# Kernel tuning notes

Hardware: AMD Instinct MI355X
Metric: run time of the kernel (lower is better)

The kernel has to match this reference:

```python
import jax, jax.numpy as jnp
import numpy as np

N_HEADS = 12


def setup_inputs() -> dict:
    key = jax.random.key(0)
    ks = jax.random.split(key, 3)
    B, N, C = 32, 1024, 768
    x = jax.random.normal(ks[0], (B, N, C), dtype=jnp.float32)
    w_qkv = jax.random.normal(ks[1], (C, 3 * C), dtype=jnp.float32) * (1.0 / np.sqrt(C))
    b_qkv = jnp.zeros((3 * C,), dtype=jnp.float32)
    w_out = jax.random.normal(ks[2], (C, C), dtype=jnp.float32) * (1.0 / np.sqrt(C))
    b_out = jnp.zeros((C,), dtype=jnp.float32)
    return {"x": x, "w_qkv": w_qkv, "b_qkv": b_qkv, "w_out": w_out, "b_out": b_out}


def reference(x, w_qkv, b_qkv, w_out, b_out):
    B, N, C = x.shape
    H = N_HEADS
    D = C // H  # head_dim
    qkv = (x @ w_qkv + b_qkv).reshape(B, N, 3, H, D)
    qkv = jnp.transpose(qkv, (2, 0, 3, 1, 4))
    q, k, v = qkv[0], qkv[1], qkv[2]
    # channel attention: k^T @ v -> (B,H,D,D), scaled by sqrt(head_dim)
    attn = jnp.einsum("bhnd,bhne->bhde", k, v) / np.sqrt(D).astype(np.float32)
    attn = jax.nn.softmax(attn, axis=-1)
    # attn @ q^T -> (B,H,D,N); swapaxes -> (B,H,N,D)
    out = jnp.einsum("bhde,bhne->bhnd", attn, q)
    # ProjOut: merge heads (B,N,C) + Dense(C)
    out = jnp.transpose(out, (0, 2, 1, 3)).reshape(B, N, C)
    return out @ w_out + b_out
```

## Files before the change

### kernel.cpp

```cpp
#include <hip/hip_runtime.h>
#include <hip/hip_bf16.h>
#include <stdint.h>
#include <stddef.h>

#define B_ 32
#define N_ 1024
#define C_ 768
#define H_ 12
#define D_ 64
#define M_ (B_*N_)
#define TC_ (3*C_)

typedef __bf16 bf16_t;
typedef __attribute__((ext_vector_type(8))) __bf16 bf16x8;
typedef __attribute__((ext_vector_type(4))) __bf16 bf16x4;
typedef __attribute__((ext_vector_type(4))) float  f32x4;
typedef __attribute__((ext_vector_type(16))) float f32x16;

#define MFMA16(a,b,c) __builtin_amdgcn_mfma_f32_16x16x32_bf16(a,b,c,0,0,0)
#define MFMA32(a,b,c) __builtin_amdgcn_mfma_f32_32x32x16_bf16(a,b,c,0,0,0)

__device__ __forceinline__ void lds_load16(const void* g, void* l) {
  __builtin_amdgcn_global_load_lds(
      (const __attribute__((address_space(1))) void*)g,
      (__attribute__((address_space(3))) void*)l, 16, 0, 0);
}

__global__ void cvt_bf16(const float* __restrict__ in, bf16_t* __restrict__ out, int n) {
  int i = (blockIdx.x * 256 + threadIdx.x) * 8;
  if (i >= n) return;
  const float4 a = *(const float4*)(in + i);
  const float4 b = *(const float4*)(in + i + 4);
  bf16x8 r;
  r[0]=(bf16_t)a.x; r[1]=(bf16_t)a.y; r[2]=(bf16_t)a.z; r[3]=(bf16_t)a.w;
  r[4]=(bf16_t)b.x; r[5]=(bf16_t)b.y; r[6]=(bf16_t)b.z; r[7]=(bf16_t)b.w;
  *(bf16x8*)(out + i) = r;
}

__global__ void transpose_cvt(const float* __restrict__ in, bf16_t* __restrict__ out,
                              int R, int Cc) {
  __shared__ float t[32][33];
  const int c0 = blockIdx.x * 32, r0 = blockIdx.y * 32;
  const int tx = threadIdx.x & 31, ty = threadIdx.x >> 5;
  #pragma unroll
  for (int k = 0; k < 4; ++k)
    t[ty + k*8][tx] = in[(size_t)(r0 + ty + k*8)*Cc + c0 + tx];
  __syncthreads();
  #pragma unroll
  for (int k = 0; k < 4; ++k)
    out[(size_t)(c0 + ty + k*8)*R + r0 + tx] = (bf16_t)t[tx][ty + k*8];
}

template<int MODE>
__global__ __launch_bounds__(256, 2)
void gemm_bt(const bf16_t* __restrict__ A, const bf16_t* __restrict__ BT,
             const float* __restrict__ bias, float* __restrict__ Cout,
             bf16_t* __restrict__ qh,
             bf16_t* __restrict__ kthi, bf16_t* __restrict__ vthi,
             int K, int nbx, size_t bt_bstride)
{
  __shared__ __align__(16) char smem[34816];
  bf16_t* As   = (bf16_t*)smem;
  bf16_t* Bs   = (bf16_t*)(smem + 8192);
  bf16_t* tile = (bf16_t*)smem;

  const int nwg = gridDim.x;
  const int cpx = nwg >> 3;
  const int bid = blockIdx.x;
  const int swz = (bid & 7) * cpx + (bid >> 3);
  const int bx  = swz % nbx;
  const int by  = swz / nbx;

  const int tid  = threadIdx.x;
  const int wave = tid >> 6;
  const int lane = tid & 63;
  const int rowBase = by * 128;
  const int colBase = bx * 128;
  const int wr = (wave >> 1) * 64;
  const int wc = (wave &  1) * 64;
  const int l31 = lane & 31;
  const int lhi = lane >> 5;
  const int xr  = (lane >> 1) & 3;
  const int r0t = tid >> 2;
  const int c0s = (((tid & 3) ^ ((tid >> 3) & 3)) << 3);

  const bf16_t* Bp = BT + (MODE == 3 ? (size_t)(rowBase >> 10) * bt_bstride : 0)
                        + (size_t)(colBase + r0t) * K + c0s;
  const bf16_t* Ap;
  if (MODE == 3) {
    const int gr = rowBase + r0t;
    Ap = A + (size_t)(gr >> 10) * (H_ * N_ * D_) + (size_t)(gr & (N_ - 1)) * D_ + c0s;
  } else {
    Ap = A + (size_t)(rowBase + r0t) * K + c0s;
  }

  f32x16 acc[2][2];
  #pragma unroll
  for (int m = 0; m < 2; ++m)
    #pragma unroll
    for (int n = 0; n < 2; ++n)
      #pragma unroll
      for (int j = 0; j < 16; ++j) acc[m][n][j] = 0.f;

  for (int k0 = 0; k0 < K; k0 += 32) {
    const bf16_t* a0;
    size_t a_half;
    if (MODE == 3) { a0 = Ap + (size_t)(k0 >> 6) * (N_ * D_) + (k0 & 63); a_half = (size_t)64 * D_; }
    else           { a0 = Ap + k0;                                        a_half = (size_t)64 * K;  }
    lds_load16(a0,              &As[wave * 512]);
    lds_load16(a0 + a_half,     &As[2048 + wave * 512]);
    lds_load16(Bp + k0,                  &Bs[wave * 512]);
    lds_load16(Bp + (size_t)64 * K + k0, &Bs[2048 + wave * 512]);
    __syncthreads();
    bf16x8 af[2][2], bfv[2][2];
    #pragma unroll
    for (int m = 0; m < 2; ++m)
      #pragma unroll
      for (int kk = 0; kk < 2; ++kk)
        af[m][kk] = *(const bf16x8*)&As[(wr + m*32 + l31)*32 + (((2*kk + lhi) ^ xr) << 3)];
    #pragma unroll
    for (int n = 0; n < 2; ++n)
      #pragma unroll
      for (int kk = 0; kk < 2; ++kk)
        bfv[n][kk] = *(const bf16x8*)&Bs[(wc + n*32 + l31)*32 + (((2*kk + lhi) ^ xr) << 3)];
    #pragma unroll
    for (int m = 0; m < 2; ++m)
      #pragma unroll
      for (int n = 0; n < 2; ++n)
        #pragma unroll
        for (int kk = 0; kk < 2; ++kk)
          acc[m][n] = MFMA32(af[m][kk], bfv[n][kk], acc[m][n]);
    __syncthreads();
  }

  if (MODE == 3) {
    #pragma unroll
    for (int n = 0; n < 2; ++n) {
      const int gc = colBase + wc + n*32 + l31;
      const float bb = bias[gc];
      #pragma unroll
      for (int m = 0; m < 2; ++m)
        #pragma unroll
        for (int g = 0; g < 4; ++g) {
          const int gr = rowBase + wr + m*32 + g*8 + lhi*4;
          #pragma unroll
          for (int j = 0; j < 4; ++j)
            Cout[(size_t)(gr + j)*C_ + gc] = acc[m][n][4*g + j] + bb;
        }
    }
  } else {
    #pragma unroll
    for (int n = 0; n < 2; ++n) {
      const int c  = wc + n*32 + l31;
      const float bb = bias[colBase + c];
      #pragma unroll
      for (int m = 0; m < 2; ++m)
        #pragma unroll
        for (int g = 0; g < 4; ++g) {
          const int r0 = wr + m*32 + g*8 + lhi*4;
          bf16x4 hv;
          hv[0]=(bf16_t)(acc[m][n][4*g+0]+bb); hv[1]=(bf16_t)(acc[m][n][4*g+1]+bb);
          hv[2]=(bf16_t)(acc[m][n][4*g+2]+bb); hv[3]=(bf16_t)(acc[m][n][4*g+3]+bb);
          *(bf16x4*)&tile[c*136 + r0] = hv;
        }
    }
    __syncthreads();
    const int s   = colBase / C_;
    const int b   = rowBase >> 10;
    const int nn0 = rowBase & (N_ - 1);
    if (s == 0) {
      const int r  = tid >> 1, ch = tid & 1;
      const int h  = (colBase >> 6) + ch;
      bf16_t* dst = qh + (((size_t)b*H_ + h)*N_ + nn0 + r)*D_;
      #pragma unroll
      for (int i0 = 0; i0 < 64; i0 += 8) {
        bf16x8 vv;
        #pragma unroll
        for (int i = 0; i < 8; ++i) vv[i] = tile[(ch*64 + i0 + i)*136 + r];
        *(bf16x8*)&dst[i0] = vv;
      }
    } else {
      const int c  = tid >> 1, rh = tid & 1;
      const int rem = colBase + c - s*C_;
      const int h = rem >> 6, d = rem & 63;
      bf16_t* dst = (s == 1 ? kthi : vthi)
                    + (((size_t)b*H_ + h)*D_ + d)*N_ + nn0 + rh*64;
      #pragma unroll
      for (int i0 = 0; i0 < 64; i0 += 8)
        *(bf16x8*)&dst[i0] = *(const bf16x8*)&tile[c*136 + rh*64 + i0];
    }
  }
}

__global__ __launch_bounds__(256, 2)
void attn_softmax_k(const bf16_t* __restrict__ kthi, const bf16_t* __restrict__ vthi,
                    bf16_t* __restrict__ attnT)
{
  __shared__ float tile[64][65];
  __shared__ float invs[64];
  const int bh = blockIdx.x;
  const int tid = threadIdx.x, wave = tid >> 6, lane = tid & 63;
  const int fr = lane & 15, fo = (lane >> 4) * 8;
  const size_t base = (size_t)bh * D_ * N_;
  f32x4 acc[4][4] = {{0.f,0.f,0.f,0.f}};
  const int k0lo = wave * 256;
  #pragma unroll 1
  for (int k0 = k0lo; k0 < k0lo + 256; k0 += 32) {
    bf16x8 ah[4], bhv[4];
    #pragma unroll
    for (int m = 0; m < 4; ++m)
      ah[m] = *(const bf16x8*)&kthi[base + (size_t)(m*16 + fr)*N_ + k0 + fo];
    #pragma unroll
    for (int n = 0; n < 4; ++n)
      bhv[n] = *(const bf16x8*)&vthi[base + (size_t)(n*16 + fr)*N_ + k0 + fo];
    #pragma unroll
    for (int m = 0; m < 4; ++m)
      #pragma unroll
      for (int n = 0; n < 4; ++n)
        acc[m][n] = MFMA16(ah[m], bhv[n], acc[m][n]);
  }
  for (int w = 0; w < 4; ++w) {
    if (wave == w) {
      #pragma unroll
      for (int m = 0; m < 4; ++m)
        #pragma unroll
        for (int n = 0; n < 4; ++n) {
          const int row = m*16 + ((lane >> 4) << 2);
          const int col = n*16 + fr;
          #pragma unroll
          for (int j = 0; j < 4; ++j) {
            if (w == 0) tile[row+j][col]  = acc[m][n][j];
            else        tile[row+j][col] += acc[m][n][j];
          }
        }
    }
    __syncthreads();
  }
  if (tid < 64) {
    float mx = -3.0e38f;
    #pragma unroll
    for (int c = 0; c < 64; ++c) mx = fmaxf(mx, tile[tid][c]);
    mx *= 0.125f;
    float ssum = 0.f;
    #pragma unroll
    for (int c = 0; c < 64; ++c) {
      const float ev = __expf(tile[tid][c]*0.125f - mx);
      tile[tid][c] = ev;
      ssum += ev;
    }
    invs[tid] = 1.0f / ssum;
  }
  __syncthreads();
  if (tid < 64) {
    bf16_t* ao = attnT + (size_t)bh * D_ * D_ + tid * D_;
    #pragma unroll
    for (int d0 = 0; d0 < 64; d0 += 8) {
      bf16x8 vv;
      #pragma unroll
      for (int i = 0; i < 8; ++i) vv[i] = (bf16_t)(tile[d0+i][tid] * invs[d0+i]);
      *(bf16x8*)&ao[d0] = vv;
    }
  }
}

__global__ __launch_bounds__(256, 2)
void compose_w2(const bf16_t* __restrict__ woutT, const bf16_t* __restrict__ attnT,
                bf16_t* __restrict__ w2t)
{
  const int jb = blockIdx.x;
  const int bh = blockIdx.y;
  const int b = bh / H_, h = bh - b*H_;
  const int tid = threadIdx.x, wave = tid >> 6, lane = tid & 63;
  const int fr = lane & 15, fo = (lane >> 4) * 8;
  const bf16_t* at = attnT + (size_t)bh * D_ * D_;
  f32x4 acc[2][4] = {{0.f,0.f,0.f,0.f}};
  #pragma unroll
  for (int kk = 0; kk < 2; ++kk) {
    bf16x8 af[2], bfv[4];
    #pragma unroll
    for (int m = 0; m < 2; ++m)
      af[m] = *(const bf16x8*)&woutT[(size_t)(jb*128 + wave*32 + m*16 + fr)*C_ + h*64 + kk*32 + fo];
    #pragma unroll
    for (int n = 0; n < 4; ++n)
      bfv[n] = *(const bf16x8*)&at[(n*16 + fr)*64 + kk*32 + fo];
    #pragma unroll
    for (int m = 0; m < 2; ++m)
      #pragma unroll
      for (int n = 0; n < 4; ++n)
        acc[m][n] = MFMA16(af[m], bfv[n], acc[m][n]);
  }
  bf16_t* wb = w2t + (size_t)b * C_ * C_;
  #pragma unroll
  for (int m = 0; m < 2; ++m) {
    const int j = jb*128 + wave*32 + m*16 + ((lane >> 4) << 2);
    #pragma unroll
    for (int n = 0; n < 4; ++n) {
      const int e = n*16 + fr;
      #pragma unroll
      for (int jj = 0; jj < 4; ++jj)
        wb[(size_t)(j + jj)*C_ + h*64 + e] = (bf16_t)acc[m][n][jj];
    }
  }
}

extern "C" void kernel_launch(void* const* d_in, const int* in_sizes, int n_in,
                              void* d_out, int out_size, void* d_ws, size_t ws_size,
                              hipStream_t stream)
{
  (void)in_sizes; (void)n_in; (void)out_size;
  const float* x     = (const float*)d_in[0];
  const float* w_qkv = (const float*)d_in[1];
  const float* b_qkv = (const float*)d_in[2];
  const float* w_out = (const float*)d_in[3];
  const float* b_out = (const float*)d_in[4];
  float* out = (float*)d_out;

  const size_t sz_xb   = (size_t)M_*C_*2;
  const size_t sz_wq   = (size_t)TC_*C_*2;
  const size_t sz_wo   = (size_t)C_*C_*2;
  const size_t sz_qh   = (size_t)B_*H_*N_*D_*2;
  const size_t sz_kv   = (size_t)B_*H_*D_*N_*2;
  const size_t sz_attn = (size_t)B_*H_*D_*D_*2;

  char* p = (char*)d_ws;
  bf16_t* xb    = (bf16_t*)p; p += sz_xb;
  bf16_t* wqkvT = (bf16_t*)p; p += sz_wq;
  bf16_t* woutT = (bf16_t*)p; p += sz_wo;
  bf16_t* qh    = (bf16_t*)p; p += sz_qh;
  bf16_t* kthi  = (bf16_t*)p; p += sz_kv;
  bf16_t* vthi  = (bf16_t*)p; p += sz_kv;
  bf16_t* attnT = (bf16_t*)p; p += sz_attn;
  const size_t base_need = (size_t)(p - (char*)d_ws);
  bf16_t* w2t = xb;

  if (ws_size < base_need) return;

  cvt_bf16<<<dim3((M_*C_)/2048), 256, 0, stream>>>(x, xb, M_*C_);
  transpose_cvt<<<dim3(TC_/32, C_/32), 256, 0, stream>>>(w_qkv, wqkvT, C_, TC_);
  transpose_cvt<<<dim3(C_/32,  C_/32), 256, 0, stream>>>(w_out, woutT, C_, C_);

  gemm_bt<1><<<dim3((TC_/128)*(M_/128)), 256, 0, stream>>>(
      xb, wqkvT, b_qkv, nullptr, qh, kthi, vthi, C_, TC_/128, 0);

  attn_softmax_k<<<dim3(B_*H_), 256, 0, stream>>>(kthi, vthi, attnT);

  compose_w2<<<dim3(C_/128, B_*H_), 256, 0, stream>>>(woutT, attnT, w2t);

  gemm_bt<3><<<dim3((C_/128)*(M_/128)), 256, 0, stream>>>(
      qh, w2t, b_out, out, nullptr, nullptr, nullptr, C_, C_/128, (size_t)C_*C_);
}
```

Baseline: 314.6 us.

## Triple-buffer GEMM LDS tiles with async prefetch and switch to 16x16 MFMA

Rewrites the shared bf16 GEMM main loop as a three-stage LDS pipeline. Two K-tiles are prefetched ahead with global_load_lds, and explicit vmcnt waits plus raw s_barrier replace the per-iteration __syncthreads pair. It also swaps 32x32x16 MFMA for 16x16x32 MFMA with a 4x4 accumulator grid, hardcodes K=768, and drops the XOR swizzle on LDS tiles. The goal is to overlap global-to-LDS loads with compute, at the cost of more LDS (48KB), possible bank conflicts from the unswizzled layout, and fragile hand-counted waitcnt logic.

```diff
diff --git a/kernel.cpp b/kernel.cpp
--- a/kernel.cpp
+++ b/kernel.cpp
@@ -10,15 +10,14 @@
 #define D_ 64
 #define M_ (B_*N_)
 #define TC_ (3*C_)
+#define NT_ 24
 
 typedef __bf16 bf16_t;
 typedef __attribute__((ext_vector_type(8))) __bf16 bf16x8;
 typedef __attribute__((ext_vector_type(4))) __bf16 bf16x4;
 typedef __attribute__((ext_vector_type(4))) float  f32x4;
-typedef __attribute__((ext_vector_type(16))) float f32x16;
 
 #define MFMA16(a,b,c) __builtin_amdgcn_mfma_f32_16x16x32_bf16(a,b,c,0,0,0)
-#define MFMA32(a,b,c) __builtin_amdgcn_mfma_f32_32x32x16_bf16(a,b,c,0,0,0)
 
 __device__ __forceinline__ void lds_load16(const void* g, void* l) {
   __builtin_amdgcn_global_load_lds(
@@ -57,11 +56,9 @@
              const float* __restrict__ bias, float* __restrict__ Cout,
              bf16_t* __restrict__ qh,
              bf16_t* __restrict__ kthi, bf16_t* __restrict__ vthi,
-             int K, int nbx, size_t bt_bstride)
+             int nbx, size_t bt_bstride)
 {
-  __shared__ __align__(16) char smem[34816];
-  bf16_t* As   = (bf16_t*)smem;
-  bf16_t* Bs   = (bf16_t*)(smem + 8192);
+  __shared__ __align__(16) char smem[49152];
   bf16_t* tile = (bf16_t*)smem;
 
   const int nwg = gridDim.x;
@@ -78,91 +75,120 @@
   const int colBase = bx * 128;
   const int wr = (wave >> 1) * 64;
   const int wc = (wave &  1) * 64;
-  const int l31 = lane & 31;
-  const int lhi = lane >> 5;
-  const int xr  = (lane >> 1) & 3;
+  const int fr = lane & 15;
+  const int fo = (lane >> 4) * 8;
   const int r0t = tid >> 2;
-  const int c0s = (((tid & 3) ^ ((tid >> 3) & 3)) << 3);
+  const int c0t = (tid & 3) * 8;
+
+  bf16_t* As[3]; bf16_t* Bs[3];
+  #pragma unroll
+  for (int i = 0; i < 3; ++i) {
+    As[i] = (bf16_t*)(smem + i * 16384);
+    Bs[i] = (bf16_t*)(smem + i * 16384 + 8192);
+  }
 
   const bf16_t* Bp = BT + (MODE == 3 ? (size_t)(rowBase >> 10) * bt_bstride : 0)
-                        + (size_t)(colBase + r0t) * K + c0s;
+                        + (size_t)(colBase + r0t) * 768 + c0t;
   const bf16_t* Ap;
+  size_t a_half;
   if (MODE == 3) {
     const int gr = rowBase + r0t;
-    Ap = A + (size_t)(gr >> 10) * (H_ * N_ * D_) + (size_t)(gr & (N_ - 1)) * D_ + c0s;
+    Ap = A + (size_t)(gr >> 10) * (H_ * N_ * D_) + (size_t)(gr & (N_ - 1)) * D_ + c0t;
+    a_half = (size_t)64 * D_;
   } else {
-    Ap = A + (size_t)(rowBase + r0t) * K + c0s;
-  }
-
-  f32x16 acc[2][2];
-  #pragma unroll
-  for (int m = 0; m < 2; ++m)
-    #pragma unroll
-    for (int n = 0; n < 2; ++n)
-      #pragma unroll
-      for (int j = 0; j < 16; ++j) acc[m][n][j] = 0.f;
-
-  for (int k0 = 0; k0 < K; k0 += 32) {
-    const bf16_t* a0;
-    size_t a_half;
-    if (MODE == 3) { a0 = Ap + (size_t)(k0 >> 6) * (N_ * D_) + (k0 & 63); a_half = (size_t)64 * D_; }
-    else           { a0 = Ap + k0;                                        a_half = (size_t)64 * K;  }
-    lds_load16(a0,              &As[wave * 512]);
-    lds_load16(a0 + a_half,     &As[2048 + wave * 512]);
-    lds_load16(Bp + k0,                  &Bs[wave * 512]);
-    lds_load16(Bp + (size_t)64 * K + k0, &Bs[2048 + wave * 512]);
-    __syncthreads();
-    bf16x8 af[2][2], bfv[2][2];
-    #pragma unroll
-    for (int m = 0; m < 2; ++m)
-      #pragma unroll
-      for (int kk = 0; kk < 2; ++kk)
-        af[m][kk] = *(const bf16x8*)&As[(wr + m*32 + l31)*32 + (((2*kk + lhi) ^ xr) << 3)];
-    #pragma unroll
-    for (int n = 0; n < 2; ++n)
-      #pragma unroll
-      for (int kk = 0; kk < 2; ++kk)
-        bfv[n][kk] = *(const bf16x8*)&Bs[(wc + n*32 + l31)*32 + (((2*kk + lhi) ^ xr) << 3)];
-    #pragma unroll
-    for (int m = 0; m < 2; ++m)
-      #pragma unroll
-      for (int n = 0; n < 2; ++n)
+    Ap = A + (size_t)(rowBase + r0t) * 768 + c0t;
+    a_half = (size_t)64 * 768;
+  }
+
+  f32x4 acc[4][4] = {{0.f,0.f,0.f,0.f}};
+
+#define STAGE(bi, t) do {                                                     \
+    const int k0_ = (t) * 32;                                                 \
+    const bf16_t* a0_ = (MODE == 3)                                           \
+        ? Ap + (size_t)(k0_ >> 6) * (N_ * D_) + (k0_ & 63)                    \
+        : Ap + k0_;                                                           \
+    lds_load16(a0_,                 As[bi] + wave * 512);                     \
+    lds_load16(a0_ + a_half,        As[bi] + 2048 + wave * 512);              \
+    lds_load16(Bp + k0_,            Bs[bi] + wave * 512);                     \
+    lds_load16(Bp + (size_t)64*768 + k0_, Bs[bi] + 2048 + wave * 512);        \
+  } while (0)
+
+#define COMPUTE(bi) do {                                                      \
+    bf16x8 af_[4], bf_[4];                                                    \
+    _Pragma("unroll")                                                         \
+    for (int m = 0; m < 4; ++m)                                               \
+      af_[m] = *(const bf16x8*)&As[bi][(wr + m*16 + fr)*32 + fo];             \
+    _Pragma("unroll")                                                         \
+    for (int n = 0; n < 4; ++n)                                               \
+      bf_[n] = *(const bf16x8*)&Bs[bi][(wc + n*16 + fr)*32 + fo];             \
+    _Pragma("unroll")                                                         \
+    for (int m = 0; m < 4; ++m)                                               \
+      _Pragma("unroll")                                                       \
+      for (int n = 0; n < 4; ++n)                                             \
+        acc[m][n] = MFMA16(af_[m], bf_[n], acc[m][n]);                        \
+  } while (0)
+
+#define WAITV(nn) do {                                                        \
+    asm volatile("s_waitcnt vmcnt(" #nn ")" ::: "memory");                    \
+    __builtin_amdgcn_sched_barrier(0);                                        \
+    __builtin_amdgcn_s_barrier();                                             \
+    __builtin_amdgcn_sched_barrier(0);                                        \
+  } while (0)
+
+#define ENDB() do {                                                           \
+    asm volatile("s_waitcnt lgkmcnt(0)" ::: "memory");                        \
+    __builtin_amdgcn_sched_barrier(0);                                        \
+    __builtin_amdgcn_s_barrier();                                             \
+    __builtin_amdgcn_sched_barrier(0);                                        \
+  } while (0)
+
+  STAGE(0, 0);
+  STAGE(1, 1);
+
+  int t = 0;
+  #pragma unroll 1
+  for (int it = 0; it < 7; ++it) {
+    STAGE(2, t+2); WAITV(8); COMPUTE(0); ENDB();
+    STAGE(0, t+3); WAITV(8); COMPUTE(1); ENDB();
+    STAGE(1, t+4); WAITV(8); COMPUTE(2); ENDB();
+    t += 3;
+  }
+  STAGE(2, 23); WAITV(8); COMPUTE(0); ENDB();
+  WAITV(4); COMPUTE(1); ENDB();
+  WAITV(0); COMPUTE(2); ENDB();
+
+#undef STAGE
+#undef COMPUTE
+#undef WAITV
+#undef ENDB
+
+  if (MODE == 3) {
+    #pragma unroll
+    for (int n = 0; n < 4; ++n) {
+      const int gc = colBase + wc + n*16 + fr;
+      const float bb = bias[gc];
+      #pragma unroll
+      for (int m = 0; m < 4; ++m) {
+        const int gr = rowBase + wr + m*16 + ((lane >> 4) << 2);
         #pragma unroll
-        for (int kk = 0; kk < 2; ++kk)
-          acc[m][n] = MFMA32(af[m][kk], bfv[n][kk], acc[m][n]);
-    __syncthreads();
-  }
-
-  if (MODE == 3) {
-    #pragma unroll
-    for (int n = 0; n < 2; ++n) {
-      const int gc = colBase + wc + n*32 + l31;
-      const float bb = bias[gc];
-      #pragma unroll
-      for (int m = 0; m < 2; ++m)
-        #pragma unroll
-        for (int g = 0; g < 4; ++g) {
-          const int gr = rowBase + wr + m*32 + g*8 + lhi*4;
-          #pragma unroll
-          for (int j = 0; j < 4; ++j)
-            Cout[(size_t)(gr + j)*C_ + gc] = acc[m][n][4*g + j] + bb;
-        }
+        for (int j = 0; j < 4; ++j)
+          Cout[(size_t)(gr + j)*C_ + gc] = acc[m][n][j] + bb;
+      }
     }
   } else {
     #pragma unroll
-    for (int n = 0; n < 2; ++n) {
-      const int c  = wc + n*32 + l31;
+    for (int n = 0; n < 4; ++n) {
+      const int c  = wc + n*16 + fr;
       const float bb = bias[colBase + c];
       #pragma unroll
-      for (int m = 0; m < 2; ++m)
-        #pragma unroll
-        for (int g = 0; g < 4; ++g) {
-          const int r0 = wr + m*32 + g*8 + lhi*4;
-          bf16x4 hv;
-          hv[0]=(bf16_t)(acc[m][n][4*g+0]+bb); hv[1]=(bf16_t)(acc[m][n][4*g+1]+bb);
-          hv[2]=(bf16_t)(acc[m][n][4*g+2]+bb); hv[3]=(bf16_t)(acc[m][n][4*g+3]+bb);
-          *(bf16x4*)&tile[c*136 + r0] = hv;
-        }
+      for (int m = 0; m < 4; ++m) {
+        const int r0 = wr + m*16 + ((lane >> 4) << 2);
+        bf16x4 hv;
+        hv[0]=(bf16_t)(acc[m][0+n][0]+bb);
+        hv[0]=(bf16_t)(acc[m][n][0]+bb); hv[1]=(bf16_t)(acc[m][n][1]+bb);
+        hv[2]=(bf16_t)(acc[m][n][2]+bb); hv[3]=(bf16_t)(acc[m][n][3]+bb);
+        *(bf16x4*)&tile[c*136 + r0] = hv;
+      }
     }
     __syncthreads();
     const int s   = colBase / C_;
@@ -340,12 +366,12 @@
   transpose_cvt<<<dim3(C_/32,  C_/32), 256, 0, stream>>>(w_out, woutT, C_, C_);
 
   gemm_bt<1><<<dim3((TC_/128)*(M_/128)), 256, 0, stream>>>(
-      xb, wqkvT, b_qkv, nullptr, qh, kthi, vthi, C_, TC_/128, 0);
+      xb, wqkvT, b_qkv, nullptr, qh, kthi, vthi, TC_/128, 0);
 
   attn_softmax_k<<<dim3(B_*H_), 256, 0, stream>>>(kthi, vthi, attnT);
 
   compose_w2<<<dim3(C_/128, B_*H_), 256, 0, stream>>>(woutT, attnT, w2t);
 
   gemm_bt<3><<<dim3((C_/128)*(M_/128)), 256, 0, stream>>>(
-      qh, w2t, b_out, out, nullptr, nullptr, nullptr, C_, C_/128, (size_t)C_*C_);
-}
+      qh, w2t, b_out, out, nullptr, nullptr, nullptr, C_/128, (size_t)C_*C_);
+}
```

Measured after the change: 295.0 us. -6.2%, faster.
